# Optimization experiments

Hardware: AMD Instinct MI355X
Metric: run time of the kernel (lower is better)

## Reference

```python
import jax, jax.numpy as jnp
import numpy as np
from jax import lax

T_MAX, BATCH, CLASSES, L_MAX = 512, 32, 1296, 64
NINF = -jnp.inf


def _align_one(logsm, label, C, R):
    """Monotonic max-probability forced alignment for one sample.
    logsm: [T, V] log-probs, label: [L] int, C=x_len (valid frames), R=label_len.
    Returns per-frame pseudo target [T] (0-padded past C)."""
    T, V = logsm.shape
    L = label.shape[0]
    rows = jnp.arange(L)
    cols = jnp.arange(T)
    # pb[i, j] = logsm[j, label[i]], restricted to the monotonic band i <= j <= C-R+i
    pb = logsm[:, label].T  # [L, T]
    band = (cols[None, :] >= rows[:, None]) & (cols[None, :] <= C - R + rows[:, None]) & (rows[:, None] < R)
    pb = jnp.where(band, pb, NINF)

    # Forward DP over time columns: dp[i,j] = max(dp[i-1,j-1], dp[i,j-1]) + pb[i,j]
    # (strict > for the diagonal move, exactly as the original numpy code).
    dp0 = jnp.where(rows == 0, pb[:, 0], NINF)

    def step(dp, pb_col):
        shifted = jnp.concatenate([jnp.full((1,), NINF, dp.dtype), dp[:-1]])
        choice = shifted > dp  # True -> came from (i-1, j-1)
        dp_new = jnp.where(choice, shifted, dp) + pb_col
        return dp_new, choice

    _, choices = lax.scan(step, dp0, pb.T[1:])  # [T-1, L] bool
    choices = jnp.concatenate([jnp.zeros((1, L), bool), choices], axis=0)  # [T, L]

    # Backtrack from (R-1, C-1); columns j >= C emit padding 0.
    def bstep(row, jc):
        j, ch = jc
        active = j < C
        tgt = jnp.where(active, label[row], 0)
        row_new = jnp.where(active, row - ch[row].astype(row.dtype), row)
        return row_new, tgt

    row0 = (R - 1).astype(jnp.int32)
    _, targets = lax.scan(bstep, row0, (jnp.arange(T), choices), reverse=True)
    return targets  # [T]


def _make_targets(logsm, label, x_len, label_len):
    # logsm: [T, B, V] -> targets [T, B]
    return jax.vmap(_align_one, in_axes=(1, 0, 0, 0))(logsm, label, x_len, label_len).T


def setup_inputs() -> dict:
    key = jax.random.key(0)
    k0, k1, k2, k3, k4 = jax.random.split(key, 5)
    pred = jax.random.normal(k0, (T_MAX, BATCH, CLASSES), jnp.float32)
    seq_pred = jax.random.normal(k1, (T_MAX, BATCH, CLASSES), jnp.float32)
    label = jax.random.randint(k2, (BATCH, L_MAX), 0, CLASSES)
    x_len = jax.random.randint(k3, (BATCH,), T_MAX // 2, T_MAX + 1)  # >= L_MAX so band is valid
    label_len = jax.random.randint(k4, (BATCH,), 8, L_MAX + 1)
    return {"pred": pred, "seq_pred": seq_pred, "label": label, "x_len": x_len, "label_len": label_len}


def reference(pred, seq_pred, label, x_len, label_len):
    T, B, V = pred.shape
    logsm_seq = jax.nn.log_softmax(seq_pred, axis=-1)
    target = _make_targets(logsm_seq, label, x_len, label_len)  # [T, B] int
    probs = jnp.exp(logsm_seq)  # softmax(seq_pred)
    conf = jnp.take_along_axis(probs, target[..., None], axis=2)[..., 0]  # [T, B]
    smooth = (1.0 - conf) / (V - 1)
    onehot = jax.nn.one_hot(target, V, dtype=pred.dtype)  # [T, B, V]
    true_dist = jnp.where(onehot > 0, conf[..., None], smooth[..., None])
    mask = (jnp.arange(T)[:, None] < x_len[None, :]).astype(pred.dtype)  # [T, B]
    ce = jnp.sum(-true_dist * jax.nn.log_softmax(pred, axis=-1), axis=-1) * mask
    return jnp.mean(ce)
```

## Files before the change

kernel.cpp:

```cpp
#include <hip/hip_runtime.h>

#define T_MAX 512
#define BATCH 32
#define CLASSES 1296
#define L_MAX 64
#define NROWS (T_MAX * BATCH)
#define NV4 (CLASSES / 4)
#define NINF (-INFINITY)

__device__ __forceinline__ float wave_sum64(float v) {
    v += __int_as_float(__builtin_amdgcn_update_dpp(0, __float_as_int(v), 0x111, 0xF, 0xF, true));
    v += __int_as_float(__builtin_amdgcn_update_dpp(0, __float_as_int(v), 0x112, 0xF, 0xF, true));
    v += __int_as_float(__builtin_amdgcn_update_dpp(0, __float_as_int(v), 0x114, 0xF, 0xF, true));
    v += __int_as_float(__builtin_amdgcn_update_dpp(0, __float_as_int(v), 0x118, 0xF, 0xF, true));
    v += __int_as_float(__builtin_amdgcn_update_dpp(0, __float_as_int(v), 0x142, 0xF, 0xF, true));
    v += __int_as_float(__builtin_amdgcn_update_dpp(0, __float_as_int(v), 0x143, 0xF, 0xF, true));
    return v;
}

__device__ __forceinline__ void glds16(const float* g, float* l) {
    __builtin_amdgcn_global_load_lds((const __attribute__((address_space(1))) void*)g,
                                     (__attribute__((address_space(3))) void*)l, 16, 0, 0);
}

__global__ __launch_bounds__(256) void seq_rowstats_kernel(
    const float* __restrict__ seqp, const int* __restrict__ label,
    float* __restrict__ lse_seq, float* __restrict__ pb, int* __restrict__ counter)
{
    int r = blockIdx.x * 4 + (threadIdx.x >> 6);
    int lane = threadIdx.x & 63;
    if (r == 0 && lane == 0) *counter = 0;
    const float* xs = seqp + (size_t)r * CLASSES;
    const float4* s4 = (const float4*)xs;

    float4 b0 = s4[lane],       b1 = s4[lane + 64],  b2 = s4[lane + 128];
    float4 b3 = s4[lane + 192], b4 = s4[lane + 256];
    float4 bt = make_float4(0.f, 0.f, 0.f, 0.f);
    if (lane < 4) bt = s4[320 + lane];
    int lab = label[((r & 31) << 6) + lane];

    float ss = __expf(b0.x) + __expf(b0.y) + __expf(b0.z) + __expf(b0.w)
             + __expf(b1.x) + __expf(b1.y) + __expf(b1.z) + __expf(b1.w)
             + __expf(b2.x) + __expf(b2.y) + __expf(b2.z) + __expf(b2.w)
             + __expf(b3.x) + __expf(b3.y) + __expf(b3.z) + __expf(b3.w)
             + __expf(b4.x) + __expf(b4.y) + __expf(b4.z) + __expf(b4.w);
    if (lane < 4)
        ss += __expf(bt.x) + __expf(bt.y) + __expf(bt.z) + __expf(bt.w);
    ss = wave_sum64(ss);

    int b = r & 31, t = r >> 5;
    pb[(((size_t)(b << 9) + t) << 6) + lane] = xs[lab];
    if (lane == 63) lse_seq[r] = __logf(ss);
}

__global__ __launch_bounds__(256) void fused_align_pred_kernel(
    const float* __restrict__ pred, const float* __restrict__ pb,
    const int* __restrict__ x_len, const int* __restrict__ label_len,
    float* __restrict__ lse_pred, float* __restrict__ sum_pred,
    int* __restrict__ tg)
{
    __shared__ float abuf[2][2048];
    __shared__ unsigned chw[1024];
    __shared__ int a_s[64];
    __shared__ int rows_s[T_MAX];

    if (blockIdx.x < 32) {
        if (threadIdx.x >= 64) return;
        int b = blockIdx.x, lane = threadIdx.x;
        int C = x_len[b], R = label_len[b];
        int limit = C - R;
        const float* pbb = pb + ((size_t)b << 15);
        int P = (C + 31) >> 5;

        float biasR = (lane < R) ? 0.f : NINF;
        bool isb0 = (lane & 15) == 0;
        const int ninf_i = 0xFF800000;

        #pragma unroll
        for (int k = 0; k < 8; ++k) glds16(pbb + (k << 8) + lane * 4, &abuf[0][k << 8]);

        float dp = NINF;
        for (int p = 0; p < P; ++p) {
            int ldp = p + 1; if (ldp >= P) ldp = P - 1;
            const float* src = pbb + ((size_t)ldp << 11);
            float* dst = abuf[(p + 1) & 1];
            #pragma unroll
            for (int k = 0; k < 8; ++k) glds16(src + (k << 8) + lane * 4, &dst[k << 8]);
            __asm__ __volatile__("s_waitcnt vmcnt(8)" ::: "memory");

            const float* bc = abuf[p & 1];
            int base = p << 5;
            unsigned w0 = 0;
            #pragma unroll
            for (int g = 0; g < 2; ++g) {
                float v[16];
                #pragma unroll
                for (int u = 0; u < 16; ++u) v[u] = bc[((g << 4) + u) * 64 + lane];
                bool general = (p == 0) || (base + (g << 4) + 15 > limit);
                #pragma unroll
                for (int u = 0; u < 16; ++u) {
                    int kk = (g << 4) + u;
                    int j = base + kk;
                    float val;
                    if (general) {
                        if (p == 0 && kk == 0) {
                            dp = (lane == 0) ? v[0] : NINF;
                            continue;
                        }
                        bool ib = (lane <= j) && (lane >= j - limit) && (lane < R);
                        val = ib ? v[u] : NINF;
                    } else {
                        val = v[u] + biasR;
                    }
                    int dpb = __float_as_int(dp);
                    int t1 = __builtin_amdgcn_update_dpp(ninf_i, dpb, 0x111, 0xF, 0xF, false);
                    int t2 = __builtin_amdgcn_update_dpp(ninf_i, dpb, 0x142, 0xF, 0xF, false);
                    float shifted = __int_as_float(isb0 ? t2 : t1);
                    bool c = shifted > dp;
                    w0 |= (c ? 1u : 0u) << kk;
                    dp = fmaxf(shifted, dp) + val;
                }
            }
            chw[(p << 6) + lane] = w0;
        }
        __asm__ __volatile__("s_waitcnt vmcnt(0)" ::: "memory");

        if (lane == 0) {
            int row = R - 1, j = C - 1;
            while (row > 0 && j >= 0) {
                unsigned word = chw[((j >> 5) << 6) + row];
                unsigned mb = (2u << (j & 31)) - 1;
                unsigned m = word & mb;
                if (m) {
                    int hb = 31 - __clz(m);
                    int aj = (j & ~31) | hb;
                    a_s[row] = aj;
                    row--; j = aj - 1;
                } else {
                    j = (j & ~31) - 1;
                }
            }
            for (int i = row; i >= 0; --i) a_s[i] = 0;
        }
        if (lane < R) {
            int a = a_s[lane];
            int bi = (lane == R - 1) ? (C - 1) : (a_s[lane + 1] - 1);
            for (int j = a; j <= bi; ++j) rows_s[j] = lane;
        }
        for (int j = lane; j < T_MAX; j += 64)
            tg[(b << 9) + j] = (j < C) ? rows_s[j] : -1;
    } else {
        int r = (blockIdx.x - 32) * 4 + (threadIdx.x >> 6);
        int lane = threadIdx.x & 63;
        const float* xp = pred + (size_t)r * CLASSES;
        const float4* p4 = (const float4*)xp;

        float4 a0 = p4[lane],       a1 = p4[lane + 64],  a2 = p4[lane + 128];
        float4 a3 = p4[lane + 192], a4 = p4[lane + 256];
        float4 at = make_float4(0.f, 0.f, 0.f, 0.f);
        if (lane < 4) at = p4[320 + lane];

        float sp = __expf(a0.x) + __expf(a0.y) + __expf(a0.z) + __expf(a0.w)
                 + __expf(a1.x) + __expf(a1.y) + __expf(a1.z) + __expf(a1.w)
                 + __expf(a2.x) + __expf(a2.y) + __expf(a2.z) + __expf(a2.w)
                 + __expf(a3.x) + __expf(a3.y) + __expf(a3.z) + __expf(a3.w)
                 + __expf(a4.x) + __expf(a4.y) + __expf(a4.z) + __expf(a4.w);
        float sx = (a0.x + a0.y + a0.z + a0.w) + (a1.x + a1.y + a1.z + a1.w)
                 + (a2.x + a2.y + a2.z + a2.w) + (a3.x + a3.y + a3.z + a3.w)
                 + (a4.x + a4.y + a4.z + a4.w);
        if (lane < 4) {
            sp += __expf(at.x) + __expf(at.y) + __expf(at.z) + __expf(at.w);
            sx += at.x + at.y + at.z + at.w;
        }
        sp = wave_sum64(sp);
        sx = wave_sum64(sx);
        if (lane == 63) {
            lse_pred[r] = __logf(sp);
            sum_pred[r] = sx;
        }
    }
}

__global__ __launch_bounds__(256) void ce_kernel(
    const float* __restrict__ pred, const int* __restrict__ label,
    const int* __restrict__ x_len,
    const float* __restrict__ lse_pred, const float* __restrict__ sum_pred,
    const float* __restrict__ lse_seq, const float* __restrict__ pb,
    const int* __restrict__ tg, float* __restrict__ partials,
    int* __restrict__ counter, float* __restrict__ out)
{
    int e = blockIdx.x * 256 + threadIdx.x;
    int t = e >> 5, b = e & 31;
    float ce = 0.f;
    if (t < x_len[b]) {
        int row = tg[(b << 9) + t];
        int tgt = label[(b << 6) + row];
        float lp = lse_pred[e];
        float S = sum_pred[e] - (float)CLASSES * lp;
        float lsp_t = pred[(size_t)e * CLASSES + tgt] - lp;
        float conf = __expf(pb[(((size_t)(b << 9) + t) << 6) + row] - lse_seq[e]);
        float smooth = (1.f - conf) * (1.f / (float)(CLASSES - 1));
        ce = -((conf - smooth) * lsp_t + smooth * S);
    }
    ce = wave_sum64(ce);
    __shared__ float sm[4];
    __shared__ int amLast;
    if ((threadIdx.x & 63) == 63) sm[threadIdx.x >> 6] = ce;
    __syncthreads();
    if (threadIdx.x == 0) {
        float p = sm[0] + sm[1] + sm[2] + sm[3];
        __hip_atomic_store(&partials[blockIdx.x], p, __ATOMIC_RELEASE, __HIP_MEMORY_SCOPE_AGENT);
        amLast = (__hip_atomic_fetch_add(counter, 1, __ATOMIC_ACQ_REL, __HIP_MEMORY_SCOPE_AGENT) == 63);
    }
    __syncthreads();
    if (amLast && threadIdx.x < 64) {
        float v = __hip_atomic_load(&partials[threadIdx.x], __ATOMIC_ACQUIRE, __HIP_MEMORY_SCOPE_AGENT);
        for (int o = 32; o; o >>= 1) v += __shfl_down(v, o, 64);
        if (threadIdx.x == 0) out[0] = v * (1.0f / (float)NROWS);
    }
}

extern "C" void kernel_launch(void* const* d_in, const int* in_sizes, int n_in,
                              void* d_out, int out_size, void* d_ws, size_t ws_size,
                              hipStream_t stream) {
    const float* pred      = (const float*)d_in[0];
    const float* seq_pred  = (const float*)d_in[1];
    const int*   label     = (const int*)d_in[2];
    const int*   x_len     = (const int*)d_in[3];
    const int*   label_len = (const int*)d_in[4];
    float* out = (float*)d_out;

    float* w = (float*)d_ws;
    float* lse_pred = w;
    float* sum_pred = w + NROWS;
    float* lse_seq  = w + 2 * NROWS;
    float* pb       = w + 3 * NROWS;
    int*   tg       = (int*)(w + 3 * NROWS + (size_t)BATCH * T_MAX * 64);
    float* partials = (float*)(tg + NROWS);
    int*   counter  = (int*)(partials + 64);

    seq_rowstats_kernel<<<NROWS / 4, 256, 0, stream>>>(seq_pred, label,
                                                       lse_seq, pb, counter);
    fused_align_pred_kernel<<<32 + NROWS / 4, 256, 0, stream>>>(pred, pb,
                                                                x_len, label_len,
                                                                lse_pred, sum_pred, tg);
    ce_kernel<<<64, 256, 0, stream>>>(pred, label, x_len,
                                      lse_pred, sum_pred, lse_seq, pb, tg,
                                      partials, counter, out);
}
```

Baseline: 217.7 us.

## Fuse seq row stats into align kernel and gather alignment inputs directly

Drops the separate seq_pred row-stats kernel and the materialized pb buffer. The 32 alignment blocks now gather their label logits straight from seq_pred, using register double-buffered panels instead of LDS async loads. All log-sum-exp row reductions for seq_pred and pred run in the same launch as the alignment, so the serial DP no longer waits for a prior kernel to finish. The cost is strided, uncoalesced global gathers inside the latency-bound DP loop and higher register pressure from two 32-float panels.

```diff
diff --git a/kernel.cpp b/kernel.cpp
--- a/kernel.cpp
+++ b/kernel.cpp
@@ -5,8 +5,8 @@
 #define CLASSES 1296
 #define L_MAX 64
 #define NROWS (T_MAX * BATCH)
-#define NV4 (CLASSES / 4)
 #define NINF (-INFINITY)
+#define COLSTRIDE (BATCH * CLASSES)
 
 __device__ __forceinline__ float wave_sum64(float v) {
     v += __int_as_float(__builtin_amdgcn_update_dpp(0, __float_as_int(v), 0x111, 0xF, 0xF, true));
@@ -18,112 +18,85 @@
     return v;
 }
 
-__device__ __forceinline__ void glds16(const float* g, float* l) {
-    __builtin_amdgcn_global_load_lds((const __attribute__((address_space(1))) void*)g,
-                                     (__attribute__((address_space(3))) void*)l, 16, 0, 0);
-}
-
-__global__ __launch_bounds__(256) void seq_rowstats_kernel(
-    const float* __restrict__ seqp, const int* __restrict__ label,
-    float* __restrict__ lse_seq, float* __restrict__ pb, int* __restrict__ counter)
+__global__ __launch_bounds__(256) void mega_kernel(
+    const float* __restrict__ pred, const float* __restrict__ seqp,
+    const int* __restrict__ label, const int* __restrict__ x_len,
+    const int* __restrict__ label_len,
+    float* __restrict__ lse_pred, float* __restrict__ sum_pred,
+    float* __restrict__ lse_seq, int* __restrict__ tg,
+    int* __restrict__ counter)
 {
-    int r = blockIdx.x * 4 + (threadIdx.x >> 6);
-    int lane = threadIdx.x & 63;
-    if (r == 0 && lane == 0) *counter = 0;
-    const float* xs = seqp + (size_t)r * CLASSES;
-    const float4* s4 = (const float4*)xs;
-
-    float4 b0 = s4[lane],       b1 = s4[lane + 64],  b2 = s4[lane + 128];
-    float4 b3 = s4[lane + 192], b4 = s4[lane + 256];
-    float4 bt = make_float4(0.f, 0.f, 0.f, 0.f);
-    if (lane < 4) bt = s4[320 + lane];
-    int lab = label[((r & 31) << 6) + lane];
-
-    float ss = __expf(b0.x) + __expf(b0.y) + __expf(b0.z) + __expf(b0.w)
-             + __expf(b1.x) + __expf(b1.y) + __expf(b1.z) + __expf(b1.w)
-             + __expf(b2.x) + __expf(b2.y) + __expf(b2.z) + __expf(b2.w)
-             + __expf(b3.x) + __expf(b3.y) + __expf(b3.z) + __expf(b3.w)
-             + __expf(b4.x) + __expf(b4.y) + __expf(b4.z) + __expf(b4.w);
-    if (lane < 4)
-        ss += __expf(bt.x) + __expf(bt.y) + __expf(bt.z) + __expf(bt.w);
-    ss = wave_sum64(ss);
-
-    int b = r & 31, t = r >> 5;
-    pb[(((size_t)(b << 9) + t) << 6) + lane] = xs[lab];
-    if (lane == 63) lse_seq[r] = __logf(ss);
-}
-
-__global__ __launch_bounds__(256) void fused_align_pred_kernel(
-    const float* __restrict__ pred, const float* __restrict__ pb,
-    const int* __restrict__ x_len, const int* __restrict__ label_len,
-    float* __restrict__ lse_pred, float* __restrict__ sum_pred,
-    int* __restrict__ tg)
-{
-    __shared__ float abuf[2][2048];
     __shared__ unsigned chw[1024];
     __shared__ int a_s[64];
     __shared__ int rows_s[T_MAX];
 
     if (blockIdx.x < 32) {
         if (threadIdx.x >= 64) return;
-        int b = blockIdx.x, lane = threadIdx.x;
-        int C = x_len[b], R = label_len[b];
-        int limit = C - R;
-        const float* pbb = pb + ((size_t)b << 15);
-        int P = (C + 31) >> 5;
-
-        float biasR = (lane < R) ? 0.f : NINF;
-        bool isb0 = (lane & 15) == 0;
+        const int b = blockIdx.x, lane = threadIdx.x;
+        if (b == 0 && lane == 0) *counter = 0;
+        const int C = x_len[b], R = label_len[b];
+        const int limit = C - R;
+        const int lab = label[(b << 6) + lane];
+        const float* gsrc = seqp + (size_t)b * CLASSES + lab;
+        const int P = (C + 31) >> 5;
+        const float biasR = (lane < R) ? 0.f : NINF;
+        const bool isb0 = (lane & 15) == 0;
         const int ninf_i = 0xFF800000;
 
-        #pragma unroll
-        for (int k = 0; k < 8; ++k) glds16(pbb + (k << 8) + lane * 4, &abuf[0][k << 8]);
-
+        float va[32], vb[32];
         float dp = NINF;
-        for (int p = 0; p < P; ++p) {
-            int ldp = p + 1; if (ldp >= P) ldp = P - 1;
-            const float* src = pbb + ((size_t)ldp << 11);
-            float* dst = abuf[(p + 1) & 1];
-            #pragma unroll
-            for (int k = 0; k < 8; ++k) glds16(src + (k << 8) + lane * 4, &dst[k << 8]);
-            __asm__ __volatile__("s_waitcnt vmcnt(8)" ::: "memory");
-
-            const float* bc = abuf[p & 1];
-            int base = p << 5;
-            unsigned w0 = 0;
-            #pragma unroll
-            for (int g = 0; g < 2; ++g) {
-                float v[16];
-                #pragma unroll
-                for (int u = 0; u < 16; ++u) v[u] = bc[((g << 4) + u) * 64 + lane];
-                bool general = (p == 0) || (base + (g << 4) + 15 > limit);
-                #pragma unroll
-                for (int u = 0; u < 16; ++u) {
-                    int kk = (g << 4) + u;
-                    int j = base + kk;
-                    float val;
-                    if (general) {
-                        if (p == 0 && kk == 0) {
-                            dp = (lane == 0) ? v[0] : NINF;
-                            continue;
-                        }
-                        bool ib = (lane <= j) && (lane >= j - limit) && (lane < R);
-                        val = ib ? v[u] : NINF;
-                    } else {
-                        val = v[u] + biasR;
-                    }
-                    int dpb = __float_as_int(dp);
-                    int t1 = __builtin_amdgcn_update_dpp(ninf_i, dpb, 0x111, 0xF, 0xF, false);
-                    int t2 = __builtin_amdgcn_update_dpp(ninf_i, dpb, 0x142, 0xF, 0xF, false);
-                    float shifted = __int_as_float(isb0 ? t2 : t1);
-                    bool c = shifted > dp;
-                    w0 |= (c ? 1u : 0u) << kk;
-                    dp = fmaxf(shifted, dp) + val;
-                }
-            }
-            chw[(p << 6) + lane] = w0;
-        }
-        __asm__ __volatile__("s_waitcnt vmcnt(0)" ::: "memory");
+
+#define LOAD_PANEL(VV, LDP) {                                                  \
+        const float* s_ = gsrc + (size_t)(LDP) * 32 * COLSTRIDE;               \
+        _Pragma("unroll")                                                      \
+        for (int u = 0; u < 32; ++u) VV[u] = s_[(size_t)u * COLSTRIDE];        \
+    }
+
+#define COMPUTE_PANEL(VV, PP) {                                                \
+        const int base = (PP) << 5;                                            \
+        unsigned w0 = 0;                                                       \
+        _Pragma("unroll")                                                      \
+        for (int g = 0; g < 2; ++g) {                                          \
+            const bool general = ((PP) == 0) || (base + (g << 4) + 15 > limit);\
+            _Pragma("unroll")                                                  \
+            for (int u = 0; u < 16; ++u) {                                     \
+                const int kk = (g << 4) + u;                                   \
+                const int j = base + kk;                                       \
+                float val;                                                     \
+                if (general) {                                                 \
+                    if ((PP) == 0 && kk == 0) {             \
+                        dp = (lane == 0) ? VV[0] : NINF;                       \
+                        continue;                                              \
+                    }                                                          \
+                    const bool ib = (lane <= j) && (lane >= j - limit) && (lane < R); \
+                    val = ib ? VV[kk] : NINF;                                  \
+                } else {                                                       \
+                    val = VV[kk] + biasR;                  \
+                }                                                              \
+                const int dpb = __float_as_int(dp);                            \
+                const int t1 = __builtin_amdgcn_update_dpp(ninf_i, dpb, 0x111, 0xF, 0xF, false);  \
+                const int t2 = __builtin_amdgcn_update_dpp(ninf_i, dpb, 0x142, 0xF, 0xF, false);  \
+                const float shifted = __int_as_float(isb0 ? t2 : t1);          \
+                const bool c = shifted > dp;               \
+                w0 |= (c ? 1u : 0u) << kk;                                     \
+                dp = fmaxf(shifted, dp) + val;             \
+            }                                                                  \
+        }                                                                      \
+        chw[((PP) << 6) + lane] = w0;                                          \
+    }
+
+        LOAD_PANEL(va, 0)
+        for (int p = 0; p < P; p += 2) {
+            int l1 = p + 1; if (l1 >= P) l1 = P - 1;
+            LOAD_PANEL(vb, l1)
+            COMPUTE_PANEL(va, p)
+            if (p + 1 >= P) break;
+            int l2 = p + 2; if (l2 >= P) l2 = P - 1;
+            LOAD_PANEL(va, l2)
+            COMPUTE_PANEL(vb, p + 1)
+        }
+#undef LOAD_PANEL
+#undef COMPUTE_PANEL
 
         if (lane == 0) {
             int row = R - 1, j = C - 1;
@@ -149,8 +122,28 @@
         }
         for (int j = lane; j < T_MAX; j += 64)
             tg[(b << 9) + j] = (j < C) ? rows_s[j] : -1;
+    } else if (blockIdx.x < 32 + NROWS / 4) {
+        int r = (blockIdx.x - 32) * 4 + (threadIdx.x >> 6);
+        int lane = threadIdx.x & 63;
+        const float* xs = seqp + (size_t)r * CLASSES;
+        const float4* s4 = (const float4*)xs;
+
+        float4 b0 = s4[lane],       b1 = s4[lane + 64],  b2 = s4[lane + 128];
+        float4 b3 = s4[lane + 192], b4 = s4[lane + 256];
+        float4 bt = make_float4(0.f, 0.f, 0.f, 0.f);
+        if (lane < 4) bt = s4[320 + lane];
+
+        float ss = __expf(b0.x) + __expf(b0.y) + __expf(b0.z) + __expf(b0.w)
+                 + __expf(b1.x) + __expf(b1.y) + __expf(b1.z) + __expf(b1.w)
+                 + __expf(b2.x) + __expf(b2.y) + __expf(b2.z) + __expf(b2.w)
+                 + __expf(b3.x) + __expf(b3.y) + __expf(b3.z) + __expf(b3.w)
+                 + __expf(b4.x) + __expf(b4.y) + __expf(b4.z) + __expf(b4.w);
+        if (lane < 4)
+            ss += __expf(bt.x) + __expf(bt.y) + __expf(bt.z) + __expf(bt.w);
+        ss = wave_sum64(ss);
+        if (lane == 63) lse_seq[r] = __logf(ss);
     } else {
-        int r = (blockIdx.x - 32) * 4 + (threadIdx.x >> 6);
+        int r = (blockIdx.x - (32 + NROWS / 4)) * 4 + (threadIdx.x >> 6);
         int lane = threadIdx.x & 63;
         const float* xp = pred + (size_t)r * CLASSES;
         const float4* p4 = (const float4*)xp;
@@ -182,10 +175,10 @@
 }
 
 __global__ __launch_bounds__(256) void ce_kernel(
-    const float* __restrict__ pred, const int* __restrict__ label,
-    const int* __restrict__ x_len,
+    const float* __restrict__ pred, const float* __restrict__ seqp,
+    const int* __restrict__ label, const int* __restrict__ x_len,
     const float* __restrict__ lse_pred, const float* __restrict__ sum_pred,
-    const float* __restrict__ lse_seq, const float* __restrict__ pb,
+    const float* __restrict__ lse_seq,
     const int* __restrict__ tg, float* __restrict__ partials,
     int* __restrict__ counter, float* __restrict__ out)
 {
@@ -198,7 +191,7 @@
         float lp = lse_pred[e];
         float S = sum_pred[e] - (float)CLASSES * lp;
         float lsp_t = pred[(size_t)e * CLASSES + tgt] - lp;
-        float conf = __expf(pb[(((size_t)(b << 9) + t) << 6) + row] - lse_seq[e]);
+        float conf = __expf(seqp[(size_t)e * CLASSES + tgt] - lse_seq[e]);
         float smooth = (1.f - conf) * (1.f / (float)(CLASSES - 1));
         ce = -((conf - smooth) * lsp_t + smooth * S);
     }
@@ -234,17 +227,15 @@
     float* lse_pred = w;
     float* sum_pred = w + NROWS;
     float* lse_seq  = w + 2 * NROWS;
-    float* pb       = w + 3 * NROWS;
-    int*   tg       = (int*)(w + 3 * NROWS + (size_t)BATCH * T_MAX * 64);
+    int*   tg       = (int*)(w + 3 * NROWS);
     float* partials = (float*)(tg + NROWS);
     int*   counter  = (int*)(partials + 64);
 
-    seq_rowstats_kernel<<<NROWS / 4, 256, 0, stream>>>(seq_pred, label,
-                                                       lse_seq, pb, counter);
-    fused_align_pred_kernel<<<32 + NROWS / 4, 256, 0, stream>>>(pred, pb,
-                                                                x_len, label_len,
-                                                                lse_pred, sum_pred, tg);
-    ce_kernel<<<64, 256, 0, stream>>>(pred, label, x_len,
-                                      lse_pred, sum_pred, lse_seq, pb, tg,
+    mega_kernel<<<32 + NROWS / 2, 256, 0, stream>>>(pred, seq_pred, label,
+                                                    x_len, label_len,
+                                                    lse_pred, sum_pred, lse_seq,
+                                                    tg, counter);
+    ce_kernel<<<64, 256, 0, stream>>>(pred, seq_pred, label, x_len,
+                                      lse_pred, sum_pred, lse_seq, tg,
                                       partials, counter, out);
 }
```

New measurement: 215.1 us. Within noise of the previous version (-1.2%).

## Deepen alignment DP prefetch to triple-buffered 64-column stages, use 512-thread blocks

Applied to the files above, without the earlier changes.

The serial alignment DP wave now streams band scores into a three-slot LDS ring. Each slot holds 64 time columns and is loaded with global_load_lds, replacing double-buffered 32-column chunks, so more loads are in flight ahead of the latency-bound recurrence. The pred row-statistics blocks become 512 threads handling 8 rows each, which halves the grid and adds an occupancy hint. The larger LDS footprint may limit how many blocks fit per CU.

```diff
diff --git a/kernel.cpp b/kernel.cpp
--- a/kernel.cpp
+++ b/kernel.cpp
@@ -5,7 +5,6 @@
 #define CLASSES 1296
 #define L_MAX 64
 #define NROWS (T_MAX * BATCH)
-#define NV4 (CLASSES / 4)
 #define NINF (-INFINITY)
 
 __device__ __forceinline__ float wave_sum64(float v) {
@@ -16,11 +15,6 @@
     v += __int_as_float(__builtin_amdgcn_update_dpp(0, __float_as_int(v), 0x142, 0xF, 0xF, true));
     v += __int_as_float(__builtin_amdgcn_update_dpp(0, __float_as_int(v), 0x143, 0xF, 0xF, true));
     return v;
-}
-
-__device__ __forceinline__ void glds16(const float* g, float* l) {
-    __builtin_amdgcn_global_load_lds((const __attribute__((address_space(1))) void*)g,
-                                     (__attribute__((address_space(3))) void*)l, 16, 0, 0);
 }
 
 __global__ __launch_bounds__(256) void seq_rowstats_kernel(
@@ -53,82 +47,95 @@
     if (lane == 63) lse_seq[r] = __logf(ss);
 }
 
-__global__ __launch_bounds__(256) void fused_align_pred_kernel(
+__global__ __launch_bounds__(512, 2) void fused_align_pred_kernel(
     const float* __restrict__ pred, const float* __restrict__ pb,
     const int* __restrict__ x_len, const int* __restrict__ label_len,
     float* __restrict__ lse_pred, float* __restrict__ sum_pred,
     int* __restrict__ tg)
 {
-    __shared__ float abuf[2][2048];
-    __shared__ unsigned chw[1024];
+    __shared__ float ring[3][64 * 64];
+    __shared__ unsigned chw[16][64];
     __shared__ int a_s[64];
     __shared__ int rows_s[T_MAX];
+    const int w = threadIdx.x >> 6, lane = threadIdx.x & 63;
 
     if (blockIdx.x < 32) {
         if (threadIdx.x >= 64) return;
-        int b = blockIdx.x, lane = threadIdx.x;
-        int C = x_len[b], R = label_len[b];
-        int limit = C - R;
+        const int b = blockIdx.x;
+        const int C = x_len[b], R = label_len[b];
+        const int limit = C - R;
         const float* pbb = pb + ((size_t)b << 15);
-        int P = (C + 31) >> 5;
-
-        float biasR = (lane < R) ? 0.f : NINF;
-        bool isb0 = (lane & 15) == 0;
+        const int P = (C + 31) >> 5;
+        const int SS = (P + 1) >> 1;
+        const float biasR = (lane < R) ? 0.f : NINF;
+        const bool isb0 = (lane & 15) == 0;
         const int ninf_i = 0xFF800000;
-
-        #pragma unroll
-        for (int k = 0; k < 8; ++k) glds16(pbb + (k << 8) + lane * 4, &abuf[0][k << 8]);
-
         float dp = NINF;
-        for (int p = 0; p < P; ++p) {
-            int ldp = p + 1; if (ldp >= P) ldp = P - 1;
-            const float* src = pbb + ((size_t)ldp << 11);
-            float* dst = abuf[(p + 1) & 1];
+
+#define STAGE(S) { const int s_ = (S); if (s_ < SS) {                          \
+        const char* src_ = (const char*)pbb + ((size_t)s_ << 14) + lane * 16;  \
+        float* dst_ = ring[s_ % 3];                                            \
+        _Pragma("unroll")                                                      \
+        for (int k = 0; k < 16; ++k)                                           \
+            __builtin_amdgcn_global_load_lds(                                  \
+                (const __attribute__((address_space(1))) void*)(src_ + (k << 10)), \
+                (__attribute__((address_space(3))) void*)(dst_ + (k << 8)), 16, 0, 0); } }
+
+        STAGE(0) STAGE(1) STAGE(2)
+        for (int s = 0; s < SS; ++s) {
+            const int rem = SS - 1 - s;
+            if (rem >= 2)      asm volatile("s_waitcnt vmcnt(32)" ::: "memory");
+            else if (rem == 1) asm volatile("s_waitcnt vmcnt(16)" ::: "memory");
+            else               asm volatile("s_waitcnt vmcnt(0)"  ::: "memory");
+            const float* sp_ = ring[s % 3];
             #pragma unroll
-            for (int k = 0; k < 8; ++k) glds16(src + (k << 8) + lane * 4, &dst[k << 8]);
-            __asm__ __volatile__("s_waitcnt vmcnt(8)" ::: "memory");
-
-            const float* bc = abuf[p & 1];
-            int base = p << 5;
-            unsigned w0 = 0;
-            #pragma unroll
-            for (int g = 0; g < 2; ++g) {
-                float v[16];
+            for (int half = 0; half < 2; ++half) {
+                const int pp = (s << 1) + half;
+                if (pp >= P) break;
+                unsigned w0 = 0;
                 #pragma unroll
-                for (int u = 0; u < 16; ++u) v[u] = bc[((g << 4) + u) * 64 + lane];
-                bool general = (p == 0) || (base + (g << 4) + 15 > limit);
-                #pragma unroll
-                for (int u = 0; u < 16; ++u) {
-                    int kk = (g << 4) + u;
-                    int j = base + kk;
-                    float val;
-                    if (general) {
-                        if (p == 0 && kk == 0) {
-                            dp = (lane == 0) ? v[0] : NINF;
-                            continue;
+                for (int g = 0; g < 2; ++g) {
+                    const int g_ = (pp << 1) + g;
+                    float v[16];
+                    #pragma unroll
+                    for (int u = 0; u < 16; ++u)
+                        v[u] = sp_[(((half << 1) + g) << 4) * 64 + (u << 6) + lane];
+                    const bool general = (g_ < 2) || (((g_ << 4) + 15) > limit);
+                    #pragma unroll
+                    for (int u = 0; u < 16; ++u) {
+                        const int kk = (g << 4) + u;
+                        const int j = (g_ << 4) + u;
+                        float val;
+                        if (general) {
+                            if (g_ == 0 && u == 0) {
+                                dp = (lane == 0) ? v[0] : NINF;
+                                continue;
+                            }
+                            const bool ib = (lane <= j) && (lane >= j - limit) && (lane < R);
+                            val = ib ? v[u] : NINF;
+                        } else {
+                            val = v[u] + biasR;
                         }
-                        bool ib = (lane <= j) && (lane >= j - limit) && (lane < R);
-                        val = ib ? v[u] : NINF;
-                    } else {
-                        val = v[u] + biasR;
+                        const int dpb = __float_as_int(dp);
+                        const int t1 = __builtin_amdgcn_update_dpp(ninf_i, dpb, 0x111, 0xF, 0xF, false);
+                        const int t2 = __builtin_amdgcn_update_dpp(ninf_i, dpb, 0x142, 0xF, 0xF, false);
+                        const float shifted = __int_as_float(isb0 ? t2 : t1);
+                        const bool c = shifted > dp;
+                        w0 |= (c ? 1u : 0u) << kk;
+                        dp = fmaxf(shifted, dp) + val;
                     }
-                    int dpb = __float_as_int(dp);
-                    int t1 = __builtin_amdgcn_update_dpp(ninf_i, dpb, 0x111, 0xF, 0xF, false);
-                    int t2 = __builtin_amdgcn_update_dpp(ninf_i, dpb, 0x142, 0xF, 0xF, false);
-                    float shifted = __int_as_float(isb0 ? t2 : t1);
-                    bool c = shifted > dp;
-                    w0 |= (c ? 1u : 0u) << kk;
-                    dp = fmaxf(shifted, dp) + val;
                 }
+                chw[pp][lane] = w0;
             }
-            chw[(p << 6) + lane] = w0;
-        }
-        __asm__ __volatile__("s_waitcnt vmcnt(0)" ::: "memory");
+            STAGE(s + 3)
+        }
+        asm volatile("s_waitcnt vmcnt(0)" ::: "memory");
+#undef STAGE
 
         if (lane == 0) {
             int row = R - 1, j = C - 1;
             while (row > 0 && j >= 0) {
-                unsigned word = chw[((j >> 5) << 6) + row];
+                unsigned word = chw[j >> 5][row];
                 unsigned mb = (2u << (j & 31)) - 1;
                 unsigned m = word & mb;
                 if (m) {
@@ -150,8 +157,7 @@
         for (int j = lane; j < T_MAX; j += 64)
             tg[(b << 9) + j] = (j < C) ? rows_s[j] : -1;
     } else {
-        int r = (blockIdx.x - 32) * 4 + (threadIdx.x >> 6);
-        int lane = threadIdx.x & 63;
+        const int r = ((blockIdx.x - 32) << 3) + w;
         const float* xp = pred + (size_t)r * CLASSES;
         const float4* p4 = (const float4*)xp;
 
@@ -230,20 +236,19 @@
     const int*   label_len = (const int*)d_in[4];
     float* out = (float*)d_out;
 
-    float* w = (float*)d_ws;
-    float* lse_pred = w;
-    float* sum_pred = w + NROWS;
-    float* lse_seq  = w + 2 * NROWS;
-    float* pb       = w + 3 * NROWS;
-    int*   tg       = (int*)(w + 3 * NROWS + (size_t)BATCH * T_MAX * 64);
+    float* ws = (float*)d_ws;
+    float* lse_pred = ws;
+    float* sum_pred = ws + NROWS;
+    float* lse_seq  = ws + 2 * NROWS;
+    float* pb       = ws + 3 * NROWS;
+    int*   tg       = (int*)(pb + (size_t)BATCH * T_MAX * 64);
     float* partials = (float*)(tg + NROWS);
     int*   counter  = (int*)(partials + 64);
 
     seq_rowstats_kernel<<<NROWS / 4, 256, 0, stream>>>(seq_pred, label,
                                                        lse_seq, pb, counter);
-    fused_align_pred_kernel<<<32 + NROWS / 4, 256, 0, stream>>>(pred, pb,
-                                                                x_len, label_len,
-                                                                lse_pred, sum_pred, tg);
+    fused_align_pred_kernel<<<32 + NROWS / 8, 512, 0, stream>>>(
+        pred, pb, x_len, label_len, lse_pred, sum_pred, tg);
     ce_kernel<<<64, 256, 0, stream>>>(pred, label, x_len,
                                       lse_pred, sum_pred, lse_seq, pb, tg,
                                       partials, counter, out);
```

After: 205.4 us. 1.06x faster.
